# Kernel tuning notes

Measured on AMD Instinct MI355X. Metric: run time of the kernel, lower is better.

## Reference

```python
import jax, jax.numpy as jnp
import numpy as np

EPSILON = 0.01  # mesh.epsilon: boundary band of the unit square


def setup_inputs() -> dict:
    key = jax.random.key(0)
    k1, k2, k3 = jax.random.split(key, 3)
    V, E, F = 50000, 150000, 128
    image = jax.random.normal(k1, (V, F), dtype=jnp.float32)
    vs = jax.random.uniform(k2, (V, 2), dtype=jnp.float32)
    edges = jax.random.randint(k3, (2, E), 0, V, dtype=jnp.int32)
    return {"image": image, "vs": vs, "edges": edges, "out_target": 25000}


def _edge_priority(image, edges):
    # features = cat(image[e0], image[e1], dim=1) -> [E, 2F]; priority = ||f||^2 per edge
    f0 = image[edges[0]]  # [E, F]
    f1 = image[edges[1]]  # [E, F]
    return jnp.sum(f0 * f0, axis=1) + jnp.sum(f1 * f1, axis=1)  # [E]


def _boundary_mask(vs, edges):
    v0 = vs[edges[0]]  # [E, 2]
    v1 = vs[edges[1]]  # [E, 2]
    def near_border(v):
        return (v[:, 0] < EPSILON) | (v[:, 0] > 1 - EPSILON) | (v[:, 1] < EPSILON) | (v[:, 1] > 1 - EPSILON)
    return near_border(v0) | near_border(v1)  # [E] bool


def reference(image, vs, edges, out_target):
    V = image.shape[0]
    sq = _edge_priority(image, edges)            # [E] float32 (heap keys)
    is_boundary = _boundary_mask(vs, edges)      # [E] bool

    # heappop order == ascending priority (ties broken by edge id, matching heapify on [value, id])
    order = jnp.argsort(sq)
    e0 = edges[0][order]
    e1 = edges[1][order]
    bnd = is_boundary[order]

    # Sequential greedy edge collapse: pop min edge; if both endpoints alive and
    # not a boundary edge, merge (kill edges[1] vertex) until vertex_count hits target.
    def step(carry, x):
        mask, count = carry
        v0, v1, b = x
        alive = mask[v0] & mask[v1]
        do = (count > out_target) & alive & (~b)
        mask = mask.at[v1].set(jnp.where(do, False, mask[v1]))
        count = count - do.astype(jnp.int32)
        return (mask, count), None

    init = (jnp.ones((V,), dtype=bool), jnp.int32(V))
    (vertex_mask, vertex_count), _ = jax.lax.scan(step, init, (e0, e1, bnd))
    return sq, vertex_mask, vertex_count
```

## Files before the change

kernel.cpp:

```cpp
#include <hip/hip_runtime.h>
#include <hip/hip_bf16.h>
#include <stdint.h>

typedef unsigned int u32;
typedef unsigned long long u64;
typedef unsigned char u8;
typedef unsigned short u16;


__global__ __launch_bounds__(256) void vnorm_kernel(const float* __restrict__ image,
                                                    float* __restrict__ nrm, int V) {
#pragma clang fp contract(off)
  int t = blockIdx.x * 256 + threadIdx.x;
  int v = t >> 1, h = t & 1;
  if (v >= V) return;
  const float4* r4 = (const float4*)(image + (size_t)v * 128) + h;
  float4 a, x;
  x = r4[0];
  a.x = x.x * x.x; a.y = x.y * x.y; a.z = x.z * x.z; a.w = x.w * x.w;
#pragma unroll
  for (int i = 1; i < 16; ++i) {
    x = r4[i * 2];
    a.x = a.x + x.x * x.x; a.y = a.y + x.y * x.y;
    a.z = a.z + x.z * x.z; a.w = a.w + x.w * x.w;
  }
  float bx = __shfl_xor(a.x, 1), by = __shfl_xor(a.y, 1);
  float bz = __shfl_xor(a.z, 1), bw = __shfl_xor(a.w, 1);
  a.x = a.x + bx; a.y = a.y + by; a.z = a.z + bz; a.w = a.w + bw;
  float r0 = a.x + a.z;
  float r1 = a.y + a.w;
  float s = r0 + r1;
  if (h == 0) nrm[v] = s;
}

__global__ __launch_bounds__(256) void edge_kernel(const float* __restrict__ nrm,
                                                   const float* __restrict__ vs,
                                                   const int* __restrict__ edges,
                                                   u64* __restrict__ keysA,
                                                   u8* __restrict__ bnd,
                                                   float* __restrict__ out_sq,
                                                   u32* __restrict__ gmm, int E) {
#pragma clang fp contract(off)
  __shared__ u32 smn[4], smx[4];
  int tid = threadIdx.x;
  int e = blockIdx.x * 256 + tid;
  u32 mn = 0xFFFFFFFFu, mx = 0u;
  if (e < E) {
    int v0 = edges[e], v1 = edges[E + e];
    float sq = nrm[v0] + nrm[v1];
    out_sq[e] = sq;
    u32 sb = __float_as_uint(sq);
    keysA[e] = ((u64)sb << 32) | (u32)e;
    float ax = vs[2 * v0], ay = vs[2 * v0 + 1];
    float bx = vs[2 * v1], by = vs[2 * v1 + 1];
    const float lo = 0.01f, hi = 0.99f;
    bool b = (ax < lo) | (ax > hi) | (ay < lo) | (ay > hi)
           | (bx < lo) | (bx > hi) | (by < lo) | (by > hi);
    bnd[e] = b ? 1 : 0;
    mn = sb; mx = sb;
  }
  int lane = tid & 63, wv = tid >> 6;
#pragma unroll
  for (int d = 32; d >= 1; d >>= 1) {
    u32 a = __shfl_xor(mn, d); mn = (a < mn) ? a : mn;
    u32 b2 = __shfl_xor(mx, d); mx = (b2 > mx) ? b2 : mx;
  }
  if (lane == 0) { smn[wv] = mn; smx[wv] = mx; }
  __syncthreads();
  if (tid == 0) {
    u32 m = smn[0], M = smx[0];
#pragma unroll
    for (int w = 1; w < 4; ++w) {
      if (smn[w] < m) m = smn[w];
      if (smx[w] > M) M = smx[w];
    }
    atomicMin(&gmm[0], m);
    atomicMax(&gmm[1], M);
  }
}

__device__ inline u32 bucket_of(u32 sb, u32 minv, u32 range) {
  return (u32)(((u64)(sb - minv) << 14) / ((u64)range + 1ull));
}

__global__ __launch_bounds__(256) void hist_kernel(const u64* __restrict__ keysA,
                                                   const u32* __restrict__ gmm,
                                                   u32* __restrict__ ghist, int E) {
  int e = blockIdx.x * 256 + threadIdx.x;
  if (e >= E) return;
  u32 minv = gmm[0], range = gmm[1] - minv;
  u32 b = bucket_of((u32)(keysA[e] >> 32), minv, range);
  atomicAdd(&ghist[b], 1u);
}

__global__ __launch_bounds__(1024) void scan16k_kernel(const u32* __restrict__ ghist,
                                                       u32* __restrict__ starts,
                                                       u32* __restrict__ cursor, int E) {
  __shared__ u32 wsum[16];
  int tid = threadIdx.x;
  int lane = tid & 63, wv = tid >> 6;
  u32 loc[16];
  u32 s = 0;
#pragma unroll
  for (int i = 0; i < 16; ++i) { loc[i] = ghist[tid * 16 + i]; s += loc[i]; }
  u32 inc = s;
#pragma unroll
  for (int d = 1; d < 64; d <<= 1) {
    u32 t = __shfl_up(inc, d);
    if (lane >= d) inc += t;
  }
  if (lane == 63) wsum[wv] = inc;
  __syncthreads();
  if (tid == 0) {
    u32 r = 0;
#pragma unroll
    for (int w = 0; w < 16; ++w) { u32 t = wsum[w]; wsum[w] = r; r += t; }
  }
  __syncthreads();
  u32 run = wsum[wv] + (inc - s);
#pragma unroll
  for (int i = 0; i < 16; ++i) {
    starts[tid * 16 + i] = run;
    cursor[tid * 16 + i] = run;
    run += loc[i];
  }
  if (tid == 0) starts[16384] = (u32)E;
}

__global__ __launch_bounds__(256) void scatter_kernel(const u64* __restrict__ keysA,
                                                      const u32* __restrict__ gmm,
                                                      u32* __restrict__ cursor,
                                                      u64* __restrict__ keysB, int E) {
  int e = blockIdx.x * 256 + threadIdx.x;
  if (e >= E) return;
  u64 key = keysA[e];
  u32 minv = gmm[0], range = gmm[1] - minv;
  u32 b = bucket_of((u32)(key >> 32), minv, range);
  u32 pos = atomicAdd(&cursor[b], 1u);
  keysB[pos] = key;
}

__global__ __launch_bounds__(256) void bucketsort_kernel(const u64* __restrict__ keysB,
                                                         const u32* __restrict__ starts,
                                                         const int* __restrict__ edges,
                                                         const u8* __restrict__ bnd,
                                                         u64* __restrict__ pack,
                                                         int E, int V, int NpadB) {
  int tid = threadIdx.x;
  int lane = tid & 63;
  int w = blockIdx.x * 4 + (tid >> 6);
  u32 start = starts[w];
  int cnt = (int)(starts[w + 1] - start);
  if (cnt > 128) cnt = 128;
  u64 k0 = (lane < cnt) ? keysB[start + lane] : ~0ull;
  u64 k1 = (64 + lane < cnt) ? keysB[start + 64 + lane] : ~0ull;
  int idx0 = lane * 2, idx1 = lane * 2 + 1;
#pragma unroll
  for (int k = 2; k <= 128; k <<= 1) {
#pragma unroll
    for (int j = 64; j >= 1; j >>= 1) {
      if (j > k / 2) continue;
      if (j >= 2) {
        int lj = j >> 1;
        u64 p0 = __shfl_xor(k0, lj);
        u64 p1 = __shfl_xor(k1, lj);
        bool keepMin0 = (((idx0 & j) == 0) == ((idx0 & k) == 0));
        k0 = keepMin0 ? (k0 < p0 ? k0 : p0) : (k0 > p0 ? k0 : p0);
        k1 = keepMin0 ? (k1 < p1 ? k1 : p1) : (k1 > p1 ? k1 : p1);
      } else {
        bool up = ((idx0 & k) == 0);
        u64 mn = (k0 < k1) ? k0 : k1;
        u64 mx = (k0 < k1) ? k1 : k0;
        k0 = up ? mn : mx;
        k1 = up ? mx : mn;
      }
    }
  }
  if (idx0 < cnt) {
    u32 id = (u32)k0;
    int vv0 = edges[id], vv1 = edges[E + id];
    pack[start + idx0] = (u64)(u32)(vv0 | (vv1 << 16)) | ((u64)bnd[id] << 32);
  }
  if (idx1 < cnt) {
    u32 id = (u32)k1;
    int vv0 = edges[id], vv1 = edges[E + id];
    pack[start + idx1] = (u64)(u32)(vv0 | (vv1 << 16)) | ((u64)bnd[id] << 32);
  }
  int g = blockIdx.x * 256 + tid;
  int i = E + g;
  if (i < NpadB) {
    u32 sv0 = (u32)V + (((u32)i & 255u) << 1);
    pack[i] = (u64)(sv0 | ((sv0 + 1) << 16)) | (1ull << 32);
  }
}

__device__ inline void lds_min_u16(u16* tarr, int idx, u16 val) {
  u32* w = (u32*)(tarr + (idx & ~1));
  int sh = (idx & 1) * 16;
  u32 old = *w;
  while (true) {
    u32 cur = (old >> sh) & 0xffffu;
    if ((u32)val >= cur) break;
    u32 nv = (old & ~(0xffffu << sh)) | ((u32)val << sh);
    u32 prev = atomicCAS(w, old, nv);
    if (prev == old) break;
    old = prev;
  }
}

#define NBAT 4096

__global__ __launch_bounds__(1024) void batch_kernel(const u64* __restrict__ pack,
                                                     const int* __restrict__ tgt,
                                                     float* __restrict__ out,
                                                     int V, int E, int NpadB) {
  __shared__ u16 tUK[50560];
  __shared__ u32 alive[1600];
  __shared__ u32 wred[65];
  __shared__ u32 misc[4];
  int tid = threadIdx.x;
  int lane = tid & 63, wv = tid >> 6;
  for (int i = tid; i < 1600; i += 1024) alive[i] = 0xFFFFFFFFu;
  for (int i = tid; i < 25280; i += 1024) ((u32*)tUK)[i] = 0xFFFFFFFFu;
  if (tid < 4) misc[tid] = 0u;
  int target = tgt[0];
  int needed = V - target; if (needed < 0) needed = 0;
  int remaining = needed;
  __syncthreads();
  int nbatch = NpadB / NBAT;
  u64 pk0 = pack[tid],        pk1 = pack[1024 + tid];
  u64 pk2 = pack[2048 + tid], pk3 = pack[3072 + tid];
  for (int b = 0; b < nbatch; ++b) {
    if (remaining <= 0) break;
    const u64* np = pack + (size_t)((b + 1 < nbatch) ? (b + 1) : b) * NBAT;
    u64 pn0 = np[tid],        pn1 = np[1024 + tid];
    u64 pn2 = np[2048 + tid], pn3 = np[3072 + tid];
#define BDEC(S) \
    int v0##S = (int)(pk##S & 0xffff), w1##S = (int)((pk##S >> 16) & 0xffff); \
    int und##S, kill##S = 0; \
    { int nb_ = (int)((pk##S >> 32) & 1); \
      int a0 = (int)((alive[v0##S >> 5] >> (v0##S & 31)) & 1); \
      int a1 = (int)((alive[w1##S >> 5] >> (w1##S & 31)) & 1); \
      und##S = a0 & a1 & (nb_ ^ 1); } \
    u32 my##S = ((u32)(S * 1024 + tid) << 1) | 1u;
    BDEC(0) BDEC(1) BDEC(2) BDEC(3)
    for (int r = 0; r < 4200; ++r) {
#define BPOST(S) if (und##S | kill##S) \
      lds_min_u16(tUK, w1##S, (u16)((((u32)(S * 1024 + tid)) << 1) | (u32)und##S));
      BPOST(0) BPOST(1) BPOST(2) BPOST(3)
      __syncthreads();
#define BDECIDE(S) \
      if (und##S) { \
        u32 b0v = (v0##S == w1##S) ? 0xFFFFu : (u32)tUK[v0##S]; \
        u32 b1v = (u32)tUK[w1##S]; \
        int ek = (int)(((b0v < my##S) & ((b0v & 1u) ^ 1u)) | \
                       ((b1v < my##S) & ((b1v & 1u) ^ 1u))); \
        int nk = (int)(b0v > my##S) & (int)(b1v == my##S) & (ek ^ 1); \
        kill##S |= nk; \
        und##S &= (nk | ek) ^ 1; \
      }
      BDECIDE(0) BDECIDE(1) BDECIDE(2) BDECIDE(3)
      u64 au = __ballot(und0 | und1 | und2 | und3);
      if (lane == 0 && au) atomicOr(&misc[r & 3], 1u);
      if (tid == 0) misc[(r + 2) & 3] = 0u;
      __syncthreads();
      tUK[w10] = 0xFFFF; tUK[w11] = 0xFFFF;
      tUK[w12] = 0xFFFF; tUK[w13] = 0xFFFF;
      u32 anyu = misc[r & 3];
      __syncthreads();
      if (anyu == 0u) break;
    }
#define BRANK(S) { u64 km = __ballot(kill##S); \
      if (lane == 0) wred[S * 16 + wv] = (u32)__popcll(km); }
    BRANK(0) BRANK(1) BRANK(2) BRANK(3)
    if (tid < 4) misc[tid] = 0u;
    __syncthreads();
    if (tid == 0) {
      u32 run = 0;
      for (int i = 0; i < 64; ++i) { u32 t2 = wred[i]; wred[i] = run; run += t2; }
      wred[64] = run;
    }
    __syncthreads();
    u32 K = wred[64];
#define BAPPLY(S) { u64 km = __ballot(kill##S); \
      if (kill##S) { \
        u32 rank = wred[S * 16 + wv] + (u32)__popcll(km & ((1ull << lane) - 1ull)); \
        if (rank < (u32)remaining) \
          atomicAnd(&alive[w1##S >> 5], ~(1u << (w1##S & 31))); } }
    BAPPLY(0) BAPPLY(1) BAPPLY(2) BAPPLY(3)
    remaining -= (int)((K < (u32)remaining) ? K : (u32)remaining);
    __syncthreads();
    pk0 = pn0; pk1 = pn1; pk2 = pn2; pk3 = pn3;
  }
  for (int i = tid; i < V; i += 1024)
    out[E + i] = ((alive[i >> 5] >> (i & 31)) & 1) ? 1.0f : 0.0f;
  if (tid == 0) out[E + V] = (float)(V - (needed - remaining));
}

extern "C" void kernel_launch(void* const* d_in, const int* in_sizes, int n_in,
                              void* d_out, int out_size, void* d_ws, size_t ws_size,
                              hipStream_t stream) {
  const float* image = (const float*)d_in[0];
  const float* vs    = (const float*)d_in[1];
  const int*   edges = (const int*)d_in[2];
  const int*   tgt   = (const int*)d_in[3];
  int V = in_sizes[1] / 2;
  int E = in_sizes[2] / 2;
  int NpadB = ((E + NBAT - 1) / NBAT) * NBAT;

  char* ws = (char*)d_ws;
  size_t o = 0;
  u64* keysA  = (u64*)(ws + o); o += (size_t)E * 8;
  u64* keysB  = (u64*)(ws + o); o += (size_t)E * 8;
  u64* pack   = (u64*)(ws + o); o += (size_t)NpadB * 8;
  float* nrm  = (float*)(ws + o); o += (size_t)V * 4;
  u8*  bnd    = (u8*)(ws + o);  o += (size_t)E;
  o = (o + 255) & ~(size_t)255;
  u32* ghist  = (u32*)(ws + o); o += 16384 * 4;
  u32* starts = (u32*)(ws + o); o += 16385 * 4;
  u32* cursor = (u32*)(ws + o); o += 16384 * 4;
  u32* gmm    = (u32*)(ws + o); o += 256;
  float* out = (float*)d_out;

  (void)hipMemsetAsync(ghist, 0, 16384 * 4, stream);
  (void)hipMemsetAsync(&gmm[0], 0xFF, 4, stream);
  (void)hipMemsetAsync(&gmm[1], 0x00, 4, stream);

  int eb = (E + 255) / 256;
  vnorm_kernel<<<dim3((2 * V + 255) / 256), dim3(256), 0, stream>>>(image, nrm, V);
  edge_kernel<<<dim3(eb), dim3(256), 0, stream>>>(nrm, vs, edges, keysA, bnd, out, gmm, E);
  hist_kernel<<<dim3(eb), dim3(256), 0, stream>>>(keysA, gmm, ghist, E);
  scan16k_kernel<<<dim3(1), dim3(1024), 0, stream>>>(ghist, starts, cursor, E);
  scatter_kernel<<<dim3(eb), dim3(256), 0, stream>>>(keysA, gmm, cursor, keysB, E);
  bucketsort_kernel<<<dim3(4096), dim3(256), 0, stream>>>(keysB, starts, edges, bnd,
                                                          pack, E, V, NpadB);
  batch_kernel<<<dim3(1), dim3(1024), 0, stream>>>(pack, tgt, out, V, E, NpadB);
}
```

Before: 237.1 us.

## Widen collapse batches to 8192 edges with 16 slots per thread

The single-block greedy collapse kernel now handles 8192 edges per batch instead of 4096. It runs 512 threads that each own 16 edge slots kept in bitmasks, where before 1024 threads each owned 4. Bigger batches mean fewer batch iterations and fewer block-wide barriers across the edge stream. The cost is more serial work per thread in each round, more registers, and possibly more conflict-resolution rounds per batch, with the round cap raised to 9000.

```diff
diff --git a/kernel.cpp b/kernel.cpp
--- a/kernel.cpp
+++ b/kernel.cpp
@@ -208,91 +208,113 @@
   }
 }
 
-#define NBAT 4096
-
-__global__ __launch_bounds__(1024) void batch_kernel(const u64* __restrict__ pack,
-                                                     const int* __restrict__ tgt,
-                                                     float* __restrict__ out,
-                                                     int V, int E, int NpadB) {
+#define TPB 512
+#define SLOTS 16
+#define NBAT 8192
+
+__global__ __launch_bounds__(512) void batch_kernel(const u64* __restrict__ pack,
+                                                    const int* __restrict__ tgt,
+                                                    float* __restrict__ out,
+                                                    int V, int E, int NpadB) {
   __shared__ u16 tUK[50560];
   __shared__ u32 alive[1600];
-  __shared__ u32 wred[65];
+  __shared__ u32 wred[129];
   __shared__ u32 misc[4];
   int tid = threadIdx.x;
   int lane = tid & 63, wv = tid >> 6;
-  for (int i = tid; i < 1600; i += 1024) alive[i] = 0xFFFFFFFFu;
-  for (int i = tid; i < 25280; i += 1024) ((u32*)tUK)[i] = 0xFFFFFFFFu;
+  for (int i = tid; i < 1600; i += TPB) alive[i] = 0xFFFFFFFFu;
+  for (int i = tid; i < 25280; i += TPB) ((u32*)tUK)[i] = 0xFFFFFFFFu;
   if (tid < 4) misc[tid] = 0u;
   int target = tgt[0];
   int needed = V - target; if (needed < 0) needed = 0;
   int remaining = needed;
   __syncthreads();
   int nbatch = NpadB / NBAT;
-  u64 pk0 = pack[tid],        pk1 = pack[1024 + tid];
-  u64 pk2 = pack[2048 + tid], pk3 = pack[3072 + tid];
+  u64 pk[SLOTS], pn[SLOTS];
+#pragma unroll
+  for (int s = 0; s < SLOTS; ++s) pk[s] = pack[s * TPB + tid];
   for (int b = 0; b < nbatch; ++b) {
     if (remaining <= 0) break;
     const u64* np = pack + (size_t)((b + 1 < nbatch) ? (b + 1) : b) * NBAT;
-    u64 pn0 = np[tid],        pn1 = np[1024 + tid];
-    u64 pn2 = np[2048 + tid], pn3 = np[3072 + tid];
-#define BDEC(S) \
-    int v0##S = (int)(pk##S & 0xffff), w1##S = (int)((pk##S >> 16) & 0xffff); \
-    int und##S, kill##S = 0; \
-    { int nb_ = (int)((pk##S >> 32) & 1); \
-      int a0 = (int)((alive[v0##S >> 5] >> (v0##S & 31)) & 1); \
-      int a1 = (int)((alive[w1##S >> 5] >> (w1##S & 31)) & 1); \
-      und##S = a0 & a1 & (nb_ ^ 1); } \
-    u32 my##S = ((u32)(S * 1024 + tid) << 1) | 1u;
-    BDEC(0) BDEC(1) BDEC(2) BDEC(3)
-    for (int r = 0; r < 4200; ++r) {
-#define BPOST(S) if (und##S | kill##S) \
-      lds_min_u16(tUK, w1##S, (u16)((((u32)(S * 1024 + tid)) << 1) | (u32)und##S));
-      BPOST(0) BPOST(1) BPOST(2) BPOST(3)
+#pragma unroll
+    for (int s = 0; s < SLOTS; ++s) pn[s] = np[s * TPB + tid];
+    u32 und = 0, kill = 0;
+#pragma unroll
+    for (int s = 0; s < SLOTS; ++s) {
+      int v0 = (int)(pk[s] & 0xffff), v1 = (int)((pk[s] >> 16) & 0xffff);
+      int nb_ = (int)((pk[s] >> 32) & 1);
+      int a0 = (int)((alive[v0 >> 5] >> (v0 & 31)) & 1);
+      int a1 = (int)((alive[v1 >> 5] >> (v1 & 31)) & 1);
+      und |= (u32)(a0 & a1 & (nb_ ^ 1)) << s;
+    }
+    for (int r = 0; r < 9000; ++r) {
+#pragma unroll
+      for (int s = 0; s < SLOTS; ++s) {
+        if ((und | kill) & (1u << s)) {
+          int v1 = (int)((pk[s] >> 16) & 0xffff);
+          u32 pos = (u32)(s * TPB + tid);
+          lds_min_u16(tUK, v1, (u16)((pos << 1) | ((und >> s) & 1)));
+        }
+      }
       __syncthreads();
-#define BDECIDE(S) \
-      if (und##S) { \
-        u32 b0v = (v0##S == w1##S) ? 0xFFFFu : (u32)tUK[v0##S]; \
-        u32 b1v = (u32)tUK[w1##S]; \
-        int ek = (int)(((b0v < my##S) & ((b0v & 1u) ^ 1u)) | \
-                       ((b1v < my##S) & ((b1v & 1u) ^ 1u))); \
-        int nk = (int)(b0v > my##S) & (int)(b1v == my##S) & (ek ^ 1); \
-        kill##S |= nk; \
-        und##S &= (nk | ek) ^ 1; \
-      }
-      BDECIDE(0) BDECIDE(1) BDECIDE(2) BDECIDE(3)
-      u64 au = __ballot(und0 | und1 | und2 | und3);
+#pragma unroll
+      for (int s = 0; s < SLOTS; ++s) {
+        if (und & (1u << s)) {
+          int v0 = (int)(pk[s] & 0xffff), v1 = (int)((pk[s] >> 16) & 0xffff);
+          u32 my = (((u32)(s * TPB + tid)) << 1) | 1u;
+          u32 b0v = (v0 == v1) ? 0xFFFFu : (u32)tUK[v0];
+          u32 b1v = (u32)tUK[v1];
+          int ek = (int)(((b0v < my) & ((b0v & 1u) ^ 1u)) |
+                         ((b1v < my) & ((b1v & 1u) ^ 1u)));
+          int nk = (int)(b0v > my) & (int)(b1v == my) & (ek ^ 1);
+          kill |= (u32)nk << s;
+          if (nk | ek) und &= ~(1u << s);
+        }
+      }
+      u64 au = __ballot(und != 0u);
       if (lane == 0 && au) atomicOr(&misc[r & 3], 1u);
       if (tid == 0) misc[(r + 2) & 3] = 0u;
       __syncthreads();
-      tUK[w10] = 0xFFFF; tUK[w11] = 0xFFFF;
-      tUK[w12] = 0xFFFF; tUK[w13] = 0xFFFF;
+#pragma unroll
+      for (int s = 0; s < SLOTS; ++s) {
+        int v1 = (int)((pk[s] >> 16) & 0xffff);
+        tUK[v1] = 0xFFFF;
+      }
       u32 anyu = misc[r & 3];
       __syncthreads();
       if (anyu == 0u) break;
     }
-#define BRANK(S) { u64 km = __ballot(kill##S); \
-      if (lane == 0) wred[S * 16 + wv] = (u32)__popcll(km); }
-    BRANK(0) BRANK(1) BRANK(2) BRANK(3)
+#pragma unroll
+    for (int s = 0; s < SLOTS; ++s) {
+      u64 km = __ballot((kill >> s) & 1);
+      if (lane == 0) wred[s * 8 + wv] = (u32)__popcll(km);
+    }
     if (tid < 4) misc[tid] = 0u;
     __syncthreads();
     if (tid == 0) {
       u32 run = 0;
-      for (int i = 0; i < 64; ++i) { u32 t2 = wred[i]; wred[i] = run; run += t2; }
-      wred[64] = run;
+      for (int i = 0; i < 128; ++i) { u32 t2 = wred[i]; wred[i] = run; run += t2; }
+      wred[128] = run;
     }
     __syncthreads();
-    u32 K = wred[64];
-#define BAPPLY(S) { u64 km = __ballot(kill##S); \
-      if (kill##S) { \
-        u32 rank = wred[S * 16 + wv] + (u32)__popcll(km & ((1ull << lane) - 1ull)); \
-        if (rank < (u32)remaining) \
-          atomicAnd(&alive[w1##S >> 5], ~(1u << (w1##S & 31))); } }
-    BAPPLY(0) BAPPLY(1) BAPPLY(2) BAPPLY(3)
+    u32 K = wred[128];
+#pragma unroll
+    for (int s = 0; s < SLOTS; ++s) {
+      u64 km = __ballot((kill >> s) & 1);
+      if ((kill >> s) & 1) {
+        u32 rank = wred[s * 8 + wv] + (u32)__popcll(km & ((1ull << lane) - 1ull));
+        if (rank < (u32)remaining) {
+          int v1 = (int)((pk[s] >> 16) & 0xffff);
+          atomicAnd(&alive[v1 >> 5], ~(1u << (v1 & 31)));
+        }
+      }
+    }
     remaining -= (int)((K < (u32)remaining) ? K : (u32)remaining);
     __syncthreads();
-    pk0 = pn0; pk1 = pn1; pk2 = pn2; pk3 = pn3;
-  }
-  for (int i = tid; i < V; i += 1024)
+#pragma unroll
+    for (int s = 0; s < SLOTS; ++s) pk[s] = pn[s];
+  }
+  for (int i = tid; i < V; i += TPB)
     out[E + i] = ((alive[i >> 5] >> (i & 31)) & 1) ? 1.0f : 0.0f;
   if (tid == 0) out[E + V] = (float)(V - (needed - remaining));
 }
@@ -334,5 +356,5 @@
   scatter_kernel<<<dim3(eb), dim3(256), 0, stream>>>(keysA, gmm, cursor, keysB, E);
   bucketsort_kernel<<<dim3(4096), dim3(256), 0, stream>>>(keysB, starts, edges, bnd,
                                                           pack, E, V, NpadB);
-  batch_kernel<<<dim3(1), dim3(1024), 0, stream>>>(pack, tgt, out, V, E, NpadB);
-}
+  batch_kernel<<<dim3(1), dim3(512), 0, stream>>>(pack, tgt, out, V, E, NpadB);
+}
```

Result: slower. 334.8 us (+41.2%).
